# Performance work log

Measured on AMD Instinct MI355X. Metric: run time of the kernel, lower is better.

Reference implementation:

```python
import jax, jax.numpy as jnp
import numpy as np

BN_EPS = 1e-5

def _sqdist(a, b):
    # a: (B,N,3), b: (B,M,3) -> (B,N,M)
    return (jnp.sum(a**2, -1)[:, :, None] + jnp.sum(b**2, -1)[:, None, :]
            - 2.0 * jnp.einsum('bnc,bmc->bnm', a, b))

def _knn_idx(pts, k):
    # smallest-k neighbor indices, (B,N,k)
    d = _sqdist(pts, pts)
    _, idx = jax.lax.top_k(-d, k)
    return idx

def _group(feat, idx):
    # feat (B,C,N), idx (B,N,K) -> (B,C,N,K)
    return jax.vmap(lambda f, i: f[:, i])(feat, idx)

def _gather_pts(pts, idx):
    # pts (B,M,C), idx (B,...) -> (B,...,C)
    return jax.vmap(lambda p, i: p[i])(pts, idx)

def _conv1(w, b, x):
    # 1x1 conv1d: w (O,C), x (B,C,N)
    return jnp.einsum('oc,bcn->bon', w, x) + b[None, :, None]

def _conv2(w, x, b=None):
    # 1x1 conv2d: w (O,C), x (B,C,N,K)
    y = jnp.einsum('oc,bcnk->bonk', w, x)
    return y if b is None else y + b[None, :, None, None]

def _bn_eval(x, gamma, beta):
    # eval-mode BatchNorm2d with running_mean=0, running_var=1
    s = gamma / jnp.sqrt(1.0 + BN_EPS)
    return x * s[None, :, None, None] + beta[None, :, None, None]

def _lgrp(x_q, x, P_anchor, map_idx, anchor_dist, lw1, lw2, lw3, k=16):
    # x_q, x: (B,n,3) -> weights (B,dim,n,k)
    d = _sqdist(x_q, x)
    _, idx = jax.lax.top_k(-d, k)                      # (B,n,k)
    neighbors = _gather_pts(x, idx)                    # (B,n,k,3)
    R1 = jnp.abs(x_q[:, :, None, :] - neighbors)       # (B,n,k,3)
    B_idx = _gather_pts(map_idx[..., None], idx)[..., 0]  # (B,n,k)
    anchorA = _gather_pts(P_anchor, map_idx)           # (B,n,3)
    anchorB = _gather_pts(P_anchor, B_idx)             # (B,n,k,3)
    dA = jnp.linalg.norm(x_q - anchorA, axis=-1)       # (B,n)
    dB = jnp.linalg.norm(neighbors - anchorB, axis=-1) # (B,n,k)
    dAB = jax.vmap(lambda ad, a, bi: ad[a[:, None], bi])(anchor_dist, map_idx, B_idx)
    R2s = dA[:, :, None] + dAB + dB                    # (B,n,k)
    R2 = jnp.broadcast_to(R2s[..., None], R1.shape)
    feats = jnp.concatenate([R1, R2], axis=-1).transpose(0, 3, 1, 2)  # (B,6,n,k)
    h = jax.nn.relu(_conv2(lw1, feats))
    h = jax.nn.relu(_conv2(lw2, h))
    return _conv2(lw3, h)                              # (B,dim,n,k)

def setup_inputs() -> dict:
    key = jax.random.key(0)
    ks = jax.random.split(key, 32)
    B, C_in, n, dim, M, k = 2, 128, 2048, 256, 128, 16
    hid_p, hid_a = 64, dim * 4
    s = 0.05
    inp = {
        'x': jax.random.normal(ks[0], (B, C_in, n), jnp.float32),
        'pos': jax.random.normal(ks[1], (B, 3, n), jnp.float32),
        'fps_idx': jax.random.randint(ks[2], (B, n), 0, n),
        'P_anchor': jax.random.normal(ks[3], (B, M, 3), jnp.float32),
        'map_idx': jax.random.randint(ks[4], (B, n), 0, M),
        'anchor_dist': jax.random.uniform(ks[5], (B, M, M), jnp.float32) * 2.0,
        'w_start': jax.random.normal(ks[6], (dim, C_in)) * s,
        'b_start': jnp.zeros((dim,), jnp.float32),
        'w_key': jax.random.normal(ks[7], (dim, dim)) * s,
        'b_key': jnp.zeros((dim,), jnp.float32),
        'w_query': jax.random.normal(ks[8], (dim, dim)) * s,
        'b_query': jnp.zeros((dim,), jnp.float32),
        'w_value': jax.random.normal(ks[9], (dim, dim)) * s,
        'b_value': jnp.zeros((dim,), jnp.float32),
        'pw1': jax.random.normal(ks[10], (hid_p, 3)) * s,
        'pb1': jnp.zeros((hid_p,), jnp.float32),
        'pg1': jnp.ones((hid_p,), jnp.float32),
        'pbt1': jnp.zeros((hid_p,), jnp.float32),
        'pw2': jax.random.normal(ks[11], (dim, hid_p)) * s,
        'pb2': jnp.zeros((dim,), jnp.float32),
        'lw1': jax.random.normal(ks[12], (32, 6)) * s,
        'lw2': jax.random.normal(ks[13], (64, 32)) * s,
        'lw3': jax.random.normal(ks[14], (dim, 64)) * s,
        'aw1': jax.random.normal(ks[15], (hid_a, dim)) * s,
        'ab1': jnp.zeros((hid_a,), jnp.float32),
        'ag1': jnp.ones((hid_a,), jnp.float32),
        'abt1': jnp.zeros((hid_a,), jnp.float32),
        'aw2': jax.random.normal(ks[16], (dim, hid_a)) * s,
        'ab2': jnp.zeros((dim,), jnp.float32),
        'w_end': jax.random.normal(ks[17], (C_in, dim)) * s,
        'b_end': jnp.zeros((C_in,), jnp.float32),
    }
    return inp

def reference(x, pos, fps_idx, P_anchor, map_idx, anchor_dist,
              w_start, b_start, w_key, b_key, w_query, b_query, w_value, b_value,
              pw1, pb1, pg1, pbt1, pw2, pb2, lw1, lw2, lw3,
              aw1, ab1, ag1, abt1, aw2, ab2, w_end, b_end):
    n_knn = 16
    identity = x
    xf = _conv1(w_start, b_start, x)                   # (B,dim,n)
    pos_f = pos.transpose(0, 2, 1)                     # (B,n,3)
    idx_knn = _knn_idx(pos_f, n_knn)                   # (B,n,k)
    key_f = _conv1(w_key, b_key, xf)
    value = _conv1(w_value, b_value, xf)
    query = _conv1(w_query, b_query, xf)
    key_g = _group(key_f, idx_knn)                     # (B,dim,n,k)
    qk_rel = query[:, :, :, None] - key_g
    pos_rel = pos[:, :, :, None] - _group(pos, idx_knn)
    f_l = _lgrp(pos_f, pos_f, P_anchor, map_idx, anchor_dist, lw1, lw2, lw3, k=16)
    # pos_mlp: conv-bn-relu-conv
    h = _bn_eval(_conv2(pw1, pos_rel, pb1), pg1, pbt1)
    pos_emb = _conv2(pw2, jax.nn.relu(h), pb2)         # (B,dim,n,k)
    # attn_mlp
    a = _bn_eval(_conv2(aw1, qk_rel + pos_emb + f_l, ab1), ag1, abt1)
    attention = _conv2(aw2, jax.nn.relu(a), ab2)
    attention = jax.nn.softmax(attention, axis=-1)
    value_e = value[:, :, :, None] + pos_emb + f_l
    agg = jnp.sum(attention * value_e, axis=-1)        # (B,dim,n)
    y = _conv1(w_end, b_end, agg)
    return y + identity
```

## Files before the change

kernel.cpp:

```cpp
#include <hip/hip_runtime.h>
#include <hip/hip_bf16.h>

typedef __hip_bfloat16 bf16;
typedef unsigned short u16;
typedef __attribute__((ext_vector_type(8))) short s8v;
typedef __attribute__((ext_vector_type(4))) float f32x4;

#define NP    2048
#define DC    256
#define MA    128
#define KNN_  16
#define LKV   768

#define MFMA_B16(a,b,c) __builtin_amdgcn_mfma_f32_16x16x32_bf16(a,b,c,0,0,0)

__device__ __forceinline__ float u2f(u16 u){ return __uint_as_float(((unsigned int)u)<<16); }
__device__ __forceinline__ u16 f2u(float f){ bf16 h=__float2bfloat16(f); u16 us; __builtin_memcpy(&us,&h,2); return us; }

__device__ __forceinline__ s8v ldpk(const u16* pk, int rb, int KS, int ks, int l){
  return *(const s8v*)(pk + (((size_t)((rb*KS + ks)*64 + l))<<3));
}
__device__ __forceinline__ s8v ldsB(const u16* base, int col, int k0, int rshift){
  int byte = ((col<<rshift) + (k0<<1)) ^ ((col&7)<<4);
  return *(const s8v*)((const char*)base + byte);
}
__device__ __forceinline__ void st2(u16* base, int col, int ch0, int rshift,
                                    float v0, float v1, float v2, float v3){
  uint2 pkv;
  pkv.x = (unsigned)f2u(v0) | ((unsigned)f2u(v1)<<16);
  pkv.y = (unsigned)f2u(v2) | ((unsigned)f2u(v3)<<16);
  int byte = ((col<<rshift) + (ch0<<1)) ^ ((col&7)<<4);
  *(uint2*)((char*)base + byte) = pkv;
}
__device__ __forceinline__ void st1(u16* base, int col, int ch, int rshift, float v){
  int byte = ((col<<rshift) + (ch<<1)) ^ ((col&7)<<4);
  *(u16*)((char*)base + byte) = f2u(v);
}
__device__ __forceinline__ void ld4s(const u16* base, int col, int ch0, int rshift, float* o){
  int byte = ((col<<rshift) + (ch0<<1)) ^ ((col&7)<<4);
  uint2 pkv = *(const uint2*)((const char*)base + byte);
  o[0] = u2f(pkv.x & 0xffff); o[1] = u2f(pkv.x>>16);
  o[2] = u2f(pkv.y & 0xffff); o[3] = u2f(pkv.y>>16);
}

template<bool XT, bool OT, bool RES>
__global__ __launch_bounds__(256) void mgemm(
    const u16* __restrict__ apk, const float* __restrict__ X,
    const float* __restrict__ bias, const float* __restrict__ resid,
    float* __restrict__ out, int M, int N, int K, int ldo)
{
  __shared__ u16 Bt[64*256];
  const int tid = threadIdx.x;
  const int w = tid>>6, l = tid&63, k = l&15, g = l>>4;
  const int n0 = blockIdx.x*64, m0 = blockIdx.y*128, bb = blockIdx.z;
  const int KS = K >> 5;
  if constexpr (!XT) {
    for (int e = tid*4; e < 64*K; e += 1024) {
      int kk = e >> 6, c = e & 63;
      float4 v = *(const float4*)(X + (size_t)bb*K*N + (size_t)kk*N + n0 + c);
      st1(Bt, c+0, kk, 9, v.x); st1(Bt, c+1, kk, 9, v.y);
      st1(Bt, c+2, kk, 9, v.z); st1(Bt, c+3, kk, 9, v.w);
    }
  } else {
    for (int e = tid*4; e < 64*256; e += 1024) {
      int c = e >> 8, kk = e & 255;
      float4 v = *(const float4*)(X + ((size_t)bb*N + n0 + c)*256 + kk);
      st2(Bt, c, kk, 9, v.x, v.y, v.z, v.w);
    }
  }
  __syncthreads();
  f32x4 acc[2][4] = {};
  const int rbase = (m0>>4) + w*2;
  for (int ks = 0; ks < KS; ks++) {
    s8v a0 = ldpk(apk, rbase,   KS, ks, l);
    s8v a1 = ldpk(apk, rbase+1, KS, ks, l);
#pragma unroll
    for (int cf = 0; cf < 4; cf++) {
      s8v bF = ldsB(Bt, cf*16 + k, ks*32 + g*8, 9);
      acc[0][cf] = MFMA_B16(a0, bF, acc[0][cf]);
      acc[1][cf] = MFMA_B16(a1, bF, acc[1][cf]);
    }
  }
#pragma unroll
  for (int ri = 0; ri < 2; ri++) {
    int mrow = m0 + w*32 + ri*16 + g*4;
#pragma unroll
    for (int r = 0; r < 4; r++) {
      int m = mrow + r;
      float bv = bias[m];
#pragma unroll
      for (int cf = 0; cf < 4; cf++) {
        int n = n0 + cf*16 + k;
        float v = acc[ri][cf][r] + bv;
        if constexpr (RES) v += resid[((size_t)bb*M + m)*N + n];
        if constexpr (OT) out[((size_t)bb*N + n)*ldo + m] = v;
        else              out[((size_t)bb*M + m)*N + n] = v;
      }
    }
  }
}

__global__ __launch_bounds__(1024) void knn_kernel(const float* __restrict__ pos, int* __restrict__ idx)
{
  __shared__ float px[NP], py[NP], pz[NP], pn[NP];
  const int tid = threadIdx.x;
  const int w = tid >> 6, l = tid & 63;
  const int bb = blockIdx.x >> 7;
  const int q0 = (blockIdx.x & 127) * 16;
  const float* pp = pos + (size_t)bb * 3 * NP;
  for (int t = tid; t < NP; t += 1024) {
    float x = pp[t], y = pp[NP + t], z = pp[2*NP + t];
    px[t] = x; py[t] = y; pz[t] = z; pn[t] = x*x + y*y + z*z;
  }
  __syncthreads();
  const int qi = q0 + w;
  const float qx = px[qi], qy = py[qi], qz = pz[qi], qn = pn[qi];
  float bd[16]; int bi[16];
#pragma unroll
  for (int t = 0; t < 16; t++) { bd[t] = 3.4e38f; bi[t] = -1; }
  float worst = 3.4e38f;
  for (int t = 0; t < 32; t++) {
    int j = t*64 + l;
    float d = qn + pn[j] - 2.f * (qx*px[j] + qy*py[j] + qz*pz[j]);
    if (__any(d < worst)) {
      float cd = (d < worst) ? d : 3.4e38f;
      int   cj = j;
#pragma unroll
      for (int s = 0; s < 16; s++) {
        bool sw = cd < bd[s];
        float od = bd[s]; int oj = bi[s];
        bd[s] = sw ? cd : od;  bi[s] = sw ? cj : oj;
        cd    = sw ? od : cd;  cj    = sw ? oj : cj;
      }
      worst = bd[15];
    }
  }
  int myj = 0;
#pragma unroll
  for (int r = 0; r < 16; r++) {
    float md = bd[0]; int mj = bi[0];
#pragma unroll
    for (int o = 1; o < 64; o <<= 1) {
      float od = __shfl_xor(md, o);
      int   oj = __shfl_xor(mj, o);
      bool tk = (od < md) || (od == md && ((unsigned)oj < (unsigned)mj));
      md = tk ? od : md;  mj = tk ? oj : mj;
    }
    if (l == r) myj = mj;
    bool win = (bi[0] == mj);
#pragma unroll
    for (int s = 0; s < 15; s++) {
      bd[s] = win ? bd[s+1] : bd[s];
      bi[s] = win ? bi[s+1] : bi[s];
    }
    bd[15] = win ? 3.4e38f : bd[15];
  }
  if (l < 16) idx[((size_t)bb * NP + qi) * KNN_ + l] = myj;
}

__global__ __launch_bounds__(256) void prep_kernel(
    const float* __restrict__ aw1, const float* __restrict__ aw2,
    const float* __restrict__ lw3, const float* __restrict__ pw2,
    const float* __restrict__ w_start, const float* __restrict__ w_key,
    const float* __restrict__ w_query, const float* __restrict__ w_value,
    const float* __restrict__ w_end,
    const float* __restrict__ b_key, const float* __restrict__ b_query,
    const float* __restrict__ b_value,
    const float* __restrict__ ag1, const float* __restrict__ ab1, const float* __restrict__ abt1,
    const float* __restrict__ pg1, const float* __restrict__ pb1, const float* __restrict__ pbt1,
    u16* __restrict__ aw1pk, u16* __restrict__ aw2pk, u16* __restrict__ wppk,
    u16* __restrict__ wstpk, u16* __restrict__ wkqvpk, u16* __restrict__ wendpk,
    float* __restrict__ sa, float* __restrict__ oa, float* __restrict__ sp,
    float* __restrict__ op_, float* __restrict__ bkqv)
{
  int i = blockIdx.x * 256 + threadIdx.x;
  const float inv = rsqrtf(1.0f + 1e-5f);
  if (i < 262144) {
    int rb = i >> 12, rem = i & 4095, ks = rem >> 9, l = (rem >> 3) & 63, j = rem & 7;
    int row = rb*16 + (l & 15), colk = ks*32 + (l >> 4)*8 + j;
    aw1pk[i] = f2u(aw1[(size_t)row*256 + colk]); return;
  }
  i -= 262144;
  if (i < 262144) {
    int rb = i >> 14, rem = i & 16383, ks = rem >> 9, l = (rem >> 3) & 63, j = rem & 7;
    int row = rb*16 + (l & 15), colk = ks*32 + (l >> 4)*8 + j;
    aw2pk[i] = f2u(aw2[(size_t)row*1024 + colk]); return;
  }
  i -= 262144;
  if (i < 32768) {
    int rb = i >> 11, rem = i & 2047, ks = rem >> 9, l = (rem >> 3) & 63, j = rem & 7;
    int row = rb*16 + (l & 15), colk = ks*32 + (l >> 4)*8 + j;
    float v = (colk < 64) ? lw3[row*64 + colk] : pw2[row*64 + (colk - 64)];
    wppk[i] = f2u(v); return;
  }
  i -= 32768;
  if (i < 32768) {
    int rb = i >> 11, rem = i & 2047, ks = rem >> 9, l = (rem >> 3) & 63, j = rem & 7;
    int row = rb*16 + (l & 15), colk = ks*32 + (l >> 4)*8 + j;
    wstpk[i] = f2u(w_start[(size_t)row*128 + colk]); return;
  }
  i -= 32768;
  if (i < 196608) {
    int rb = i >> 12, rem = i & 4095, ks = rem >> 9, l = (rem >> 3) & 63, j = rem & 7;
    int row = rb*16 + (l & 15), colk = ks*32 + (l >> 4)*8 + j;
    float v = (row < 256) ? w_key[(size_t)row*256 + colk]
            : (row < 512) ? w_query[(size_t)(row-256)*256 + colk]
                          : w_value[(size_t)(row-512)*256 + colk];
    wkqvpk[i] = f2u(v); return;
  }
  i -= 196608;
  if (i < 32768) {
    int rb = i >> 12, rem = i & 4095, ks = rem >> 9, l = (rem >> 3) & 63, j = rem & 7;
    int row = rb*16 + (l & 15), colk = ks*32 + (l >> 4)*8 + j;
    wendpk[i] = f2u(w_end[(size_t)row*256 + colk]); return;
  }
  i -= 32768;
  if (i < 1024) { float s_ = ag1[i]*inv; sa[i] = s_; oa[i] = ab1[i]*s_ + abt1[i]; return; }
  i -= 1024;
  if (i < 64)  { float s_ = pg1[i]*inv; sp[i] = s_; op_[i] = pb1[i]*s_ + pbt1[i]; return; }
  i -= 64;
  if (i < 768) {
    bkqv[i] = (i < 256) ? b_key[i] : (i < 512) ? b_query[i-256] : b_value[i-512];
  }
}

__global__ __launch_bounds__(256, 2) void fused_attn(
    const float* __restrict__ kqv, const int* __restrict__ knn_idx,
    const float* __restrict__ pos, const int* __restrict__ map_idx,
    const float* __restrict__ P_anchor, const float* __restrict__ adist,
    const float* __restrict__ lw1f, const float* __restrict__ lw2f, const float* __restrict__ pw1f,
    const float* __restrict__ spv, const float* __restrict__ opv, const float* __restrict__ pb2f,
    const u16* __restrict__ aw1pk, const float* __restrict__ sav, const float* __restrict__ oav,
    const u16* __restrict__ aw2pk, const u16* __restrict__ wppk, const float* __restrict__ ab2f,
    float* __restrict__ aggT)
{
  __shared__ __align__(16) char smem[49152];
  u16*   s_t   = (u16*)smem;
  u16*   hid_t = (u16*)(smem + 32768);
  float* fFEAT = (float*)smem;
  float* fPREL = (float*)(smem + 1632);
  u16*   fH1   = (u16*) (smem + 2448);
  __shared__ int s_idx[4][16];

  const int tid = threadIdx.x;
  const int w = tid >> 6, l = tid & 63;
  const int k = l & 15, g = l >> 4;
  const int p0 = blockIdx.x * 4;
  const int b = p0 >> 11, pi0 = p0 & 2047;
  const int pi = pi0 + w;
  const int col_w = w*16 + k;

  const float* kqvB = kqv + (size_t)b * NP * LKV;

  if (l < 16) {
    int kk = l;
    int j = knn_idx[((size_t)(b*NP) + pi) * KNN_ + kk];
    s_idx[w][kk] = j;
    const float* pp = pos + (size_t)b * 3 * NP;
    float qx = pp[pi], qy = pp[NP+pi], qz = pp[2*NP+pi];
    float nx = pp[j],  ny = pp[NP+j],  nz = pp[2*NP+j];
    float r1x = qx-nx, r1y = qy-ny, r1z = qz-nz;
    fPREL[(w*3+0)*17+kk] = r1x; fPREL[(w*3+1)*17+kk] = r1y; fPREL[(w*3+2)*17+kk] = r1z;
    int mi = map_idx[b*NP + pi];
    int bj = map_idx[b*NP + j];
    const float* pa = P_anchor + (size_t)b * MA * 3;
    float ax = pa[mi*3], ay = pa[mi*3+1], az = pa[mi*3+2];
    float bx = pa[bj*3], by = pa[bj*3+1], bz = pa[bj*3+2];
    float dA = sqrtf((qx-ax)*(qx-ax)+(qy-ay)*(qy-ay)+(qz-az)*(qz-az));
    float dB = sqrtf((nx-bx)*(nx-bx)+(ny-by)*(ny-by)+(nz-bz)*(nz-bz));
    float dAB = adist[(size_t)b*MA*MA + mi*MA + bj];
    float r2 = dA + dAB + dB;
    fFEAT[(w*6+0)*17+kk] = fabsf(r1x); fFEAT[(w*6+1)*17+kk] = fabsf(r1y);
    fFEAT[(w*6+2)*17+kk] = fabsf(r1z);
    fFEAT[(w*6+3)*17+kk] = r2; fFEAT[(w*6+4)*17+kk] = r2; fFEAT[(w*6+5)*17+kk] = r2;
  }
  __syncthreads();

  {
    float f0=fFEAT[(w*6+0)*17+k], f1=fFEAT[(w*6+1)*17+k], f2=fFEAT[(w*6+2)*17+k],
          f3=fFEAT[(w*6+3)*17+k], f4=fFEAT[(w*6+4)*17+k], f5=fFEAT[(w*6+5)*17+k];
#pragma unroll
    for (int jj = 0; jj < 8; jj++) {
      int h = g*8 + jj;
      const float* wp = lw1f + h*6;
      float v = wp[0]*f0 + wp[1]*f1 + wp[2]*f2 + wp[3]*f3 + wp[4]*f4 + wp[5]*f5;
      fH1[(w*32+h)*17+k] = f2u(fmaxf(v, 0.f));
    }
  }
  __syncthreads();

  {
    float hr[32];
#pragma unroll
    for (int t = 0; t < 32; t++) hr[t] = u2f(fH1[(w*32+t)*17+k]);
#pragma unroll
    for (int jj = 0; jj < 16; jj++) {
      int h = g*16 + jj;
      const float4* wp = (const float4*)(lw2f + h*32);
      float a = 0.f;
#pragma unroll
      for (int t4 = 0; t4 < 8; t4++) {
        float4 wv = wp[t4];
        a += wv.x*hr[t4*4] + wv.y*hr[t4*4+1] + wv.z*hr[t4*4+2] + wv.w*hr[t4*4+3];
      }
      st1(hid_t, col_w, h, 8, fmaxf(a, 0.f));
    }
    float pr0 = fPREL[(w*3+0)*17+k], pr1 = fPREL[(w*3+1)*17+k], pr2 = fPREL[(w*3+2)*17+k];
#pragma unroll
    for (int jj = 0; jj < 16; jj++) {
      int h = g*16 + jj;
      float d = pw1f[h*3]*pr0 + pw1f[h*3+1]*pr1 + pw1f[h*3+2]*pr2;
      st1(hid_t, col_w, 64 + h, 8, fmaxf(d*spv[h] + opv[h], 0.f));
    }
  }
  __syncthreads();

  {
    f32x4 accs[4][4];
#pragma unroll
    for (int fr = 0; fr < 4; fr++) {
      int ch0 = w*64 + fr*16 + g*4;
      const float4 p4 = *(const float4*)(pb2f + ch0);
#pragma unroll
      for (int fc = 0; fc < 4; fc++) {
        int j = s_idx[fc][k];
        const float4 q4 = *(const float4*)(kqvB + (size_t)(pi0 + fc)*LKV + 256 + ch0);
        const float4 k4 = *(const float4*)(kqvB + (size_t)j*LKV + ch0);
        accs[fr][fc][0] = q4.x - k4.x + p4.x;
        accs[fr][fc][1] = q4.y - k4.y + p4.y;
        accs[fr][fc][2] = q4.z - k4.z + p4.z;
        accs[fr][fc][3] = q4.w - k4.w + p4.w;
      }
    }
#pragma unroll
    for (int ks = 0; ks < 4; ks++) {
      s8v aF[4];
#pragma unroll
      for (int fr = 0; fr < 4; fr++) aF[fr] = ldpk(wppk, w*4 + fr, 4, ks, l);
#pragma unroll
      for (int fc = 0; fc < 4; fc++) {
        s8v bF = ldsB(hid_t, fc*16 + k, ks*32 + g*8, 8);
#pragma unroll
        for (int fr = 0; fr < 4; fr++) accs[fr][fc] = MFMA_B16(aF[fr], bF, accs[fr][fc]);
      }
    }
#pragma unroll
    for (int fr = 0; fr < 4; fr++)
#pragma unroll
      for (int fc = 0; fc < 4; fc++)
        st2(s_t, fc*16 + k, w*64 + fr*16 + g*4, 9,
            accs[fr][fc][0], accs[fr][fc][1], accs[fr][fc][2], accs[fr][fc][3]);
  }
  __syncthreads();

  f32x4 acc2[4][4];
#pragma unroll
  for (int fr = 0; fr < 4; fr++) {
    const float4 a4 = *(const float4*)(ab2f + w*64 + fr*16 + g*4);
#pragma unroll
    for (int fc = 0; fc < 4; fc++) {
      acc2[fr][fc][0] = a4.x; acc2[fr][fc][1] = a4.y;
      acc2[fr][fc][2] = a4.z; acc2[fr][fc][3] = a4.w;
    }
  }

  for (int c = 0; c < 8; c++) {
    f32x4 acc1[2][4] = {};
    int rb0 = c*8 + w*2;
#pragma unroll
    for (int ks = 0; ks < 8; ks++) {
      s8v a0 = ldpk(aw1pk, rb0,     8, ks, l);
      s8v a1 = ldpk(aw1pk, rb0 + 1, 8, ks, l);
#pragma unroll
      for (int cf = 0; cf < 4; cf++) {
        s8v bF = ldsB(s_t, cf*16 + k, ks*32 + g*8, 9);
        acc1[0][cf] = MFMA_B16(a0, bF, acc1[0][cf]);
        acc1[1][cf] = MFMA_B16(a1, bF, acc1[1][cf]);
      }
    }
    __syncthreads();
#pragma unroll
    for (int ri = 0; ri < 2; ri++) {
      int hl = w*32 + ri*16 + g*4;
      int hg = c*128 + hl;
      const float4 sc = *(const float4*)(sav + hg);
      const float4 of = *(const float4*)(oav + hg);
#pragma unroll
      for (int cf = 0; cf < 4; cf++) {
        float v0 = fmaxf(acc1[ri][cf][0]*sc.x + of.x, 0.f);
        float v1 = fmaxf(acc1[ri][cf][1]*sc.y + of.y, 0.f);
        float v2 = fmaxf(acc1[ri][cf][2]*sc.z + of.z, 0.f);
        float v3 = fmaxf(acc1[ri][cf][3]*sc.w + of.w, 0.f);
        st2(hid_t, cf*16 + k, hl, 8, v0, v1, v2, v3);
      }
    }
    __syncthreads();
#pragma unroll
    for (int ks = 0; ks < 4; ks++) {
      s8v aF[4];
#pragma unroll
      for (int rf = 0; rf < 4; rf++) aF[rf] = ldpk(aw2pk, w*4 + rf, 32, c*4 + ks, l);
#pragma unroll
      for (int cf = 0; cf < 4; cf++) {
        s8v bF = ldsB(hid_t, cf*16 + k, ks*32 + g*8, 8);
#pragma unroll
        for (int rf = 0; rf < 4; rf++) acc2[rf][cf] = MFMA_B16(aF[rf], bF, acc2[rf][cf]);
      }
    }
  }

#pragma unroll
  for (int fc = 0; fc < 4; fc++) {
    int j = s_idx[fc][k];
    const float* qp = kqvB + (size_t)(pi0 + fc)*LKV + 256;
    const float* kp = kqvB + (size_t)j*LKV;
    const float* vp = kqvB + (size_t)(pi0 + fc)*LKV + 512;
#pragma unroll
    for (int fr = 0; fr < 4; fr++) {
      int ch0 = w*64 + fr*16 + g*4;
      float q4[4], k4[4], v4[4], s4[4], res[4];
      *(float4*)q4 = *(const float4*)(qp + ch0);
      *(float4*)k4 = *(const float4*)(kp + ch0);
      *(float4*)v4 = *(const float4*)(vp + ch0);
      ld4s(s_t, fc*16 + k, ch0, 9, s4);
#pragma unroll
      for (int r = 0; r < 4; r++) {
        float a = acc2[fr][fc][r];
        float m = a;
        m = fmaxf(m, __shfl_xor(m, 1, 16)); m = fmaxf(m, __shfl_xor(m, 2, 16));
        m = fmaxf(m, __shfl_xor(m, 4, 16)); m = fmaxf(m, __shfl_xor(m, 8, 16));
        float ex = __expf(a - m);
        float se = ex;
        se += __shfl_xor(se, 1, 16); se += __shfl_xor(se, 2, 16);
        se += __shfl_xor(se, 4, 16); se += __shfl_xor(se, 8, 16);
        float watt = ex / se;
        float ve = v4[r] - q4[r] + k4[r] + s4[r];
        float cc = watt * ve;
        cc += __shfl_xor(cc, 1, 16); cc += __shfl_xor(cc, 2, 16);
        cc += __shfl_xor(cc, 4, 16); cc += __shfl_xor(cc, 8, 16);
        res[r] = cc;
      }
      if (k == 0)
        *(float4*)(aggT + ((size_t)(b*NP) + pi0 + fc)*DC + ch0) =
            make_float4(res[0], res[1], res[2], res[3]);
    }
  }
}

extern "C" void kernel_launch(void* const* d_in, const int* in_sizes, int n_in,
                              void* d_out, int out_size, void* d_ws, size_t ws_size,
                              hipStream_t stream)
{
  const float* x        = (const float*)d_in[0];
  const float* pos      = (const float*)d_in[1];
  const float* P_anchor = (const float*)d_in[3];
  const int*   map_idx  = (const int*)  d_in[4];
  const float* adist    = (const float*)d_in[5];
  const float* w_start  = (const float*)d_in[6];
  const float* b_start  = (const float*)d_in[7];
  const float* w_key    = (const float*)d_in[8];
  const float* b_key    = (const float*)d_in[9];
  const float* w_query  = (const float*)d_in[10];
  const float* b_query  = (const float*)d_in[11];
  const float* w_value  = (const float*)d_in[12];
  const float* b_value  = (const float*)d_in[13];
  const float* pw1      = (const float*)d_in[14];
  const float* pb1      = (const float*)d_in[15];
  const float* pg1      = (const float*)d_in[16];
  const float* pbt1     = (const float*)d_in[17];
  const float* pw2      = (const float*)d_in[18];
  const float* pb2      = (const float*)d_in[19];
  const float* lw1      = (const float*)d_in[20];
  const float* lw2      = (const float*)d_in[21];
  const float* lw3      = (const float*)d_in[22];
  const float* aw1      = (const float*)d_in[23];
  const float* ab1      = (const float*)d_in[24];
  const float* ag1      = (const float*)d_in[25];
  const float* abt1     = (const float*)d_in[26];
  const float* aw2      = (const float*)d_in[27];
  const float* ab2      = (const float*)d_in[28];
  const float* w_end    = (const float*)d_in[29];
  const float* b_end    = (const float*)d_in[30];

  if (ws_size < (size_t)4672384 * 4) return;

  float* ws     = (float*)d_ws;
  float* xf     = ws + 0;
  float* aggT   = ws + 0;
  float* kqvT   = ws + 1048576;
  u16*   aw1pk  = (u16*)(ws + 4194304);
  u16*   aw2pk  = (u16*)(ws + 4325376);
  u16*   wppk   = (u16*)(ws + 4456448);
  u16*   wstpk  = (u16*)(ws + 4472832);
  u16*   wkqvpk = (u16*)(ws + 4489216);
  u16*   wendpk = (u16*)(ws + 4587520);
  float* sa     = ws + 4603904;
  float* oa     = ws + 4604928;
  float* sp     = ws + 4605952;
  float* op_    = ws + 4606016;
  float* bkqv   = ws + 4606080;
  int*   knn_i  = (int*)(ws + 4606848);

  prep_kernel<<<3208, 256, 0, stream>>>(aw1, aw2, lw3, pw2,
      w_start, w_key, w_query, w_value, w_end, b_key, b_query, b_value,
      ag1, ab1, abt1, pg1, pb1, pbt1,
      aw1pk, aw2pk, wppk, wstpk, wkqvpk, wendpk, sa, oa, sp, op_, bkqv);

  mgemm<false, false, false><<<dim3(32, 2, 2), 256, 0, stream>>>(
      wstpk, x, b_start, nullptr, xf, 256, NP, 128, 0);

  knn_kernel<<<256, 1024, 0, stream>>>(pos, knn_i);

  mgemm<false, true, false><<<dim3(32, 6, 2), 256, 0, stream>>>(
      wkqvpk, xf, bkqv, nullptr, kqvT, 768, NP, 256, LKV);

  fused_attn<<<1024, 256, 0, stream>>>(kqvT, knn_i,
      pos, map_idx, P_anchor, adist,
      lw1, lw2, pw1, sp, op_, pb2,
      aw1pk, sa, oa, aw2pk, wppk, ab2, aggT);

  mgemm<true, false, true><<<dim3(32, 1, 2), 256, 0, stream>>>(
      wendpk, aggT, b_end, x, (float*)d_out, 128, NP, 256, 0);
}
```

Baseline: 241.9 us.

## Shrink LDS footprint by halving hidden tile and splitting pos-MLP staging

The hidden LDS buffer shrinks from 128 to 64 columns of width: the lgrp hidden and the pos_mlp hidden are now staged one after another with an extra barrier, and the attn_mlp chunk loop runs 16 chunks of 64 instead of 8 of 128. The shared knn index array is dropped and indices are reloaded from global memory. Total LDS falls from 48KB plus the index array to 40KB, which could let more blocks fit per CU. The cost is twice as many barriers in the main loop, less A-fragment reuse per MFMA step, and extra global index loads.

```diff
diff --git a/kernel.cpp b/kernel.cpp
--- a/kernel.cpp
+++ b/kernel.cpp
@@ -234,13 +234,12 @@
     const u16* __restrict__ aw2pk, const u16* __restrict__ wppk, const float* __restrict__ ab2f,
     float* __restrict__ aggT)
 {
-  __shared__ __align__(16) char smem[49152];
+  __shared__ __align__(16) char smem[40960];
   u16*   s_t   = (u16*)smem;
   u16*   hid_t = (u16*)(smem + 32768);
   float* fFEAT = (float*)smem;
   float* fPREL = (float*)(smem + 1632);
   u16*   fH1   = (u16*) (smem + 2448);
-  __shared__ int s_idx[4][16];
 
   const int tid = threadIdx.x;
   const int w = tid >> 6, l = tid & 63;
@@ -251,11 +250,11 @@
   const int col_w = w*16 + k;
 
   const float* kqvB = kqv + (size_t)b * NP * LKV;
+  const int* knnB = knn_idx + ((size_t)b * NP) * KNN_;
 
   if (l < 16) {
     int kk = l;
-    int j = knn_idx[((size_t)(b*NP) + pi) * KNN_ + kk];
-    s_idx[w][kk] = j;
+    int j = knnB[(size_t)pi * KNN_ + kk];
     const float* pp = pos + (size_t)b * 3 * NP;
     float qx = pp[pi], qy = pp[NP+pi], qz = pp[2*NP+pi];
     float nx = pp[j],  ny = pp[NP+j],  nz = pp[2*NP+j];
@@ -303,27 +302,20 @@
         float4 wv = wp[t4];
         a += wv.x*hr[t4*4] + wv.y*hr[t4*4+1] + wv.z*hr[t4*4+2] + wv.w*hr[t4*4+3];
       }
-      st1(hid_t, col_w, h, 8, fmaxf(a, 0.f));
-    }
-    float pr0 = fPREL[(w*3+0)*17+k], pr1 = fPREL[(w*3+1)*17+k], pr2 = fPREL[(w*3+2)*17+k];
-#pragma unroll
-    for (int jj = 0; jj < 16; jj++) {
-      int h = g*16 + jj;
-      float d = pw1f[h*3]*pr0 + pw1f[h*3+1]*pr1 + pw1f[h*3+2]*pr2;
-      st1(hid_t, col_w, 64 + h, 8, fmaxf(d*spv[h] + opv[h], 0.f));
-    }
-  }
-  __syncthreads();
-
+      st1(hid_t, col_w, h, 7, fmaxf(a, 0.f));
+    }
+  }
+  __syncthreads();
+
+  f32x4 accs[4][4];
   {
-    f32x4 accs[4][4];
 #pragma unroll
     for (int fr = 0; fr < 4; fr++) {
       int ch0 = w*64 + fr*16 + g*4;
       const float4 p4 = *(const float4*)(pb2f + ch0);
 #pragma unroll
       for (int fc = 0; fc < 4; fc++) {
-        int j = s_idx[fc][k];
+        int j = knnB[(size_t)(pi0 + fc) * KNN_ + k];
         const float4 q4 = *(const float4*)(kqvB + (size_t)(pi0 + fc)*LKV + 256 + ch0);
         const float4 k4 = *(const float4*)(kqvB + (size_t)j*LKV + ch0);
         accs[fr][fc][0] = q4.x - k4.x + p4.x;
@@ -333,13 +325,40 @@
       }
     }
 #pragma unroll
-    for (int ks = 0; ks < 4; ks++) {
+    for (int ks = 0; ks < 2; ks++) {
       s8v aF[4];
 #pragma unroll
       for (int fr = 0; fr < 4; fr++) aF[fr] = ldpk(wppk, w*4 + fr, 4, ks, l);
 #pragma unroll
       for (int fc = 0; fc < 4; fc++) {
-        s8v bF = ldsB(hid_t, fc*16 + k, ks*32 + g*8, 8);
+        s8v bF = ldsB(hid_t, fc*16 + k, ks*32 + g*8, 7);
+#pragma unroll
+        for (int fr = 0; fr < 4; fr++) accs[fr][fc] = MFMA_B16(aF[fr], bF, accs[fr][fc]);
+      }
+    }
+  }
+  __syncthreads();
+
+  {
+    float pr0 = fPREL[(w*3+0)*17+k], pr1 = fPREL[(w*3+1)*17+k], pr2 = fPREL[(w*3+2)*17+k];
+#pragma unroll
+    for (int jj = 0; jj < 16; jj++) {
+      int h = g*16 + jj;
+      float d = pw1f[h*3]*pr0 + pw1f[h*3+1]*pr1 + pw1f[h*3+2]*pr2;
+      st1(hid_t, col_w, h, 7, fmaxf(d*spv[h] + opv[h], 0.f));
+    }
+  }
+  __syncthreads();
+
+  {
+#pragma unroll
+    for (int ks = 0; ks < 2; ks++) {
+      s8v aF[4];
+#pragma unroll
+      for (int fr = 0; fr < 4; fr++) aF[fr] = ldpk(wppk, w*4 + fr, 4, 2 + ks, l);
+#pragma unroll
+      for (int fc = 0; fc < 4; fc++) {
+        s8v bF = ldsB(hid_t, fc*16 + k, ks*32 + g*8, 7);
 #pragma unroll
         for (int fr = 0; fr < 4; fr++) accs[fr][fc] = MFMA_B16(aF[fr], bF, accs[fr][fc]);
       }
@@ -364,45 +383,42 @@
     }
   }
 
-  for (int c = 0; c < 8; c++) {
-    f32x4 acc1[2][4] = {};
-    int rb0 = c*8 + w*2;
+  for (int c = 0; c < 16; c++) {
+    f32x4 acc1[4] = {};
+    const int rb = c*4 + w;
 #pragma unroll
     for (int ks = 0; ks < 8; ks++) {
-      s8v a0 = ldpk(aw1pk, rb0,     8, ks, l);
-      s8v a1 = ldpk(aw1pk, rb0 + 1, 8, ks, l);
+      s8v a0 = ldpk(aw1pk, rb, 8, ks, l);
 #pragma unroll
       for (int cf = 0; cf < 4; cf++) {
         s8v bF = ldsB(s_t, cf*16 + k, ks*32 + g*8, 9);
-        acc1[0][cf] = MFMA_B16(a0, bF, acc1[0][cf]);
-        acc1[1][cf] = MFMA_B16(a1, bF, acc1[1][cf]);
+        acc1[cf] = MFMA_B16(a0, bF, acc1[cf]);
       }
     }
     __syncthreads();
-#pragma unroll
-    for (int ri = 0; ri < 2; ri++) {
-      int hl = w*32 + ri*16 + g*4;
-      int hg = c*128 + hl;
+    {
+      int hl = w*16 + g*4;
+      int hg = rb*16 + g*4;
       const float4 sc = *(const float4*)(sav + hg);
       const float4 of = *(const float4*)(oav + hg);
 #pragma unroll
       for (int cf = 0; cf < 4; cf++) {
-        float v0 = fmaxf(acc1[ri][cf][0]*sc.x + of.x, 0.f);
-        float v1 = fmaxf(acc1[ri][cf][1]*sc.y + of.y, 0.f);
-        float v2 = fmaxf(acc1[ri][cf][2]*sc.z + of.z, 0.f);
-        float v3 = fmaxf(acc1[ri][cf][3]*sc.w + of.w, 0.f);
-        st2(hid_t, cf*16 + k, hl, 8, v0, v1, v2, v3);
+        float v0 = fmaxf(acc1[cf][0]*sc.x + of.x, 0.f);
+        float v1 = fmaxf(acc1[cf][1]*sc.y + of.y, 0.f);
+        float v2 = fmaxf(acc1[cf][2]*sc.z + of.z, 0.f);
+        float v3 = fmaxf(acc1[cf][3]*sc.w + of.w, 0.f);
+        st2(hid_t, cf*16 + k, hl, 7, v0, v1, v2, v3);
       }
     }
     __syncthreads();
 #pragma unroll
-    for (int ks = 0; ks < 4; ks++) {
+    for (int ks = 0; ks < 2; ks++) {
       s8v aF[4];
 #pragma unroll
-      for (int rf = 0; rf < 4; rf++) aF[rf] = ldpk(aw2pk, w*4 + rf, 32, c*4 + ks, l);
+      for (int rf = 0; rf < 4; rf++) aF[rf] = ldpk(aw2pk, w*4 + rf, 32, c*2 + ks, l);
 #pragma unroll
       for (int cf = 0; cf < 4; cf++) {
-        s8v bF = ldsB(hid_t, cf*16 + k, ks*32 + g*8, 8);
+        s8v bF = ldsB(hid_t, cf*16 + k, ks*32 + g*8, 7);
 #pragma unroll
         for (int rf = 0; rf < 4; rf++) acc2[rf][cf] = MFMA_B16(aF[rf], bF, acc2[rf][cf]);
       }
@@ -411,7 +427,7 @@
 
 #pragma unroll
   for (int fc = 0; fc < 4; fc++) {
-    int j = s_idx[fc][k];
+    int j = knnB[(size_t)(pi0 + fc) * KNN_ + k];
     const float* qp = kqvB + (size_t)(pi0 + fc)*LKV + 256;
     const float* kp = kqvB + (size_t)j*LKV;
     const float* vp = kqvB + (size_t)(pi0 + fc)*LKV + 512;
```

New measurement: 234.8 us. 1.03x faster.

## Switch fused attention MLP GEMMs to 32x32x16 bf16 MFMA tiles

Applied to the files above, without the earlier changes.

Repacks the aw1, aw2 and lw3/pw2 weights for the 32x32x16 MFMA operand layout and rewrites all three in-kernel GEMMs to use 32x32 tiles. Each wave now computes 2x2 32x32 fragments instead of 4x4 16x16 ones, which cuts the MFMA instruction count and the B-operand LDS reads per FLOP. The hidden chunk grows to 256 rows per outer iteration (4 iterations instead of 8), so the hidden LDS buffer doubles and shared memory rises to 64KB. Neighbor indices are reread from global memory instead of a shared array. The larger LDS footprint may reduce the number of blocks resident per CU.

```diff
diff --git a/kernel.cpp b/kernel.cpp
--- a/kernel.cpp
+++ b/kernel.cpp
@@ -5,6 +5,7 @@
 typedef unsigned short u16;
 typedef __attribute__((ext_vector_type(8))) short s8v;
 typedef __attribute__((ext_vector_type(4))) float f32x4;
+typedef __attribute__((ext_vector_type(16))) float f32x16;
 
 #define NP    2048
 #define DC    256
@@ -13,6 +14,7 @@
 #define LKV   768
 
 #define MFMA_B16(a,b,c) __builtin_amdgcn_mfma_f32_16x16x32_bf16(a,b,c,0,0,0)
+#define MFMA32(a,b,c)   __builtin_amdgcn_mfma_f32_32x32x16_bf16(a,b,c,0,0,0)
 
 __device__ __forceinline__ float u2f(u16 u){ return __uint_as_float(((unsigned int)u)<<16); }
 __device__ __forceinline__ u16 f2u(float f){ bf16 h=__float2bfloat16(f); u16 us; __builtin_memcpy(&us,&h,2); return us; }
@@ -176,20 +178,20 @@
   int i = blockIdx.x * 256 + threadIdx.x;
   const float inv = rsqrtf(1.0f + 1e-5f);
   if (i < 262144) {
-    int rb = i >> 12, rem = i & 4095, ks = rem >> 9, l = (rem >> 3) & 63, j = rem & 7;
-    int row = rb*16 + (l & 15), colk = ks*32 + (l >> 4)*8 + j;
+    int j = i & 7, l = (i >> 3) & 63, ks = (i >> 9) & 15, rb = i >> 13;
+    int row = rb*32 + (l & 31), colk = ks*16 + (l >> 5)*8 + j;
     aw1pk[i] = f2u(aw1[(size_t)row*256 + colk]); return;
   }
   i -= 262144;
   if (i < 262144) {
-    int rb = i >> 14, rem = i & 16383, ks = rem >> 9, l = (rem >> 3) & 63, j = rem & 7;
-    int row = rb*16 + (l & 15), colk = ks*32 + (l >> 4)*8 + j;
+    int j = i & 7, l = (i >> 3) & 63, ks = (i >> 9) & 63, rb = i >> 15;
+    int row = rb*32 + (l & 31), colk = ks*16 + (l >> 5)*8 + j;
     aw2pk[i] = f2u(aw2[(size_t)row*1024 + colk]); return;
   }
   i -= 262144;
   if (i < 32768) {
-    int rb = i >> 11, rem = i & 2047, ks = rem >> 9, l = (rem >> 3) & 63, j = rem & 7;
-    int row = rb*16 + (l & 15), colk = ks*32 + (l >> 4)*8 + j;
+    int j = i & 7, l = (i >> 3) & 63, ks = (i >> 9) & 7, rb = i >> 12;
+    int row = rb*32 + (l & 31), colk = ks*16 + (l >> 5)*8 + j;
     float v = (colk < 64) ? lw3[row*64 + colk] : pw2[row*64 + (colk - 64)];
     wppk[i] = f2u(v); return;
   }
@@ -234,28 +236,28 @@
     const u16* __restrict__ aw2pk, const u16* __restrict__ wppk, const float* __restrict__ ab2f,
     float* __restrict__ aggT)
 {
-  __shared__ __align__(16) char smem[49152];
+  __shared__ __align__(16) char smem[65536];
   u16*   s_t   = (u16*)smem;
   u16*   hid_t = (u16*)(smem + 32768);
   float* fFEAT = (float*)smem;
   float* fPREL = (float*)(smem + 1632);
   u16*   fH1   = (u16*) (smem + 2448);
-  __shared__ int s_idx[4][16];
 
   const int tid = threadIdx.x;
   const int w = tid >> 6, l = tid & 63;
   const int k = l & 15, g = l >> 4;
+  const int c32 = l & 31, h = l >> 5;
   const int p0 = blockIdx.x * 4;
   const int b = p0 >> 11, pi0 = p0 & 2047;
   const int pi = pi0 + w;
   const int col_w = w*16 + k;
 
   const float* kqvB = kqv + (size_t)b * NP * LKV;
+  const int* knnB = knn_idx + ((size_t)b * NP) * KNN_;
 
   if (l < 16) {
     int kk = l;
-    int j = knn_idx[((size_t)(b*NP) + pi) * KNN_ + kk];
-    s_idx[w][kk] = j;
+    int j = knnB[(size_t)pi * KNN_ + kk];
     const float* pp = pos + (size_t)b * 3 * NP;
     float qx = pp[pi], qy = pp[NP+pi], qz = pp[2*NP+pi];
     float nx = pp[j],  ny = pp[NP+j],  nz = pp[2*NP+j];
@@ -281,10 +283,10 @@
           f3=fFEAT[(w*6+3)*17+k], f4=fFEAT[(w*6+4)*17+k], f5=fFEAT[(w*6+5)*17+k];
 #pragma unroll
     for (int jj = 0; jj < 8; jj++) {
-      int h = g*8 + jj;
-      const float* wp = lw1f + h*6;
+      int hh = g*8 + jj;
+      const float* wp = lw1f + hh*6;
       float v = wp[0]*f0 + wp[1]*f1 + wp[2]*f2 + wp[3]*f3 + wp[4]*f4 + wp[5]*f5;
-      fH1[(w*32+h)*17+k] = f2u(fmaxf(v, 0.f));
+      fH1[(w*32+hh)*17+k] = f2u(fmaxf(v, 0.f));
     }
   }
   __syncthreads();
@@ -295,137 +297,152 @@
     for (int t = 0; t < 32; t++) hr[t] = u2f(fH1[(w*32+t)*17+k]);
 #pragma unroll
     for (int jj = 0; jj < 16; jj++) {
-      int h = g*16 + jj;
-      const float4* wp = (const float4*)(lw2f + h*32);
+      int hh = g*16 + jj;
+      const float4* wp = (const float4*)(lw2f + hh*32);
       float a = 0.f;
 #pragma unroll
       for (int t4 = 0; t4 < 8; t4++) {
         float4 wv = wp[t4];
         a += wv.x*hr[t4*4] + wv.y*hr[t4*4+1] + wv.z*hr[t4*4+2] + wv.w*hr[t4*4+3];
       }
-      st1(hid_t, col_w, h, 8, fmaxf(a, 0.f));
+      st1(hid_t, col_w, hh, 9, fmaxf(a, 0.f));
     }
     float pr0 = fPREL[(w*3+0)*17+k], pr1 = fPREL[(w*3+1)*17+k], pr2 = fPREL[(w*3+2)*17+k];
 #pragma unroll
     for (int jj = 0; jj < 16; jj++) {
-      int h = g*16 + jj;
-      float d = pw1f[h*3]*pr0 + pw1f[h*3+1]*pr1 + pw1f[h*3+2]*pr2;
-      st1(hid_t, col_w, 64 + h, 8, fmaxf(d*spv[h] + opv[h], 0.f));
+      int hh = g*16 + jj;
+      float d = pw1f[hh*3]*pr0 + pw1f[hh*3+1]*pr1 + pw1f[hh*3+2]*pr2;
+      st1(hid_t, col_w, 64 + hh, 9, fmaxf(d*spv[hh] + opv[hh], 0.f));
     }
   }
   __syncthreads();
 
   {
-    f32x4 accs[4][4];
-#pragma unroll
-    for (int fr = 0; fr < 4; fr++) {
-      int ch0 = w*64 + fr*16 + g*4;
-      const float4 p4 = *(const float4*)(pb2f + ch0);
-#pragma unroll
-      for (int fc = 0; fc < 4; fc++) {
-        int j = s_idx[fc][k];
-        const float4 q4 = *(const float4*)(kqvB + (size_t)(pi0 + fc)*LKV + 256 + ch0);
-        const float4 k4 = *(const float4*)(kqvB + (size_t)j*LKV + ch0);
-        accs[fr][fc][0] = q4.x - k4.x + p4.x;
-        accs[fr][fc][1] = q4.y - k4.y + p4.y;
-        accs[fr][fc][2] = q4.z - k4.z + p4.z;
-        accs[fr][fc][3] = q4.w - k4.w + p4.w;
-      }
-    }
-#pragma unroll
-    for (int ks = 0; ks < 4; ks++) {
-      s8v aF[4];
-#pragma unroll
-      for (int fr = 0; fr < 4; fr++) aF[fr] = ldpk(wppk, w*4 + fr, 4, ks, l);
-#pragma unroll
-      for (int fc = 0; fc < 4; fc++) {
-        s8v bF = ldsB(hid_t, fc*16 + k, ks*32 + g*8, 8);
-#pragma unroll
-        for (int fr = 0; fr < 4; fr++) accs[fr][fc] = MFMA_B16(aF[fr], bF, accs[fr][fc]);
-      }
-    }
-#pragma unroll
-    for (int fr = 0; fr < 4; fr++)
-#pragma unroll
-      for (int fc = 0; fc < 4; fc++)
-        st2(s_t, fc*16 + k, w*64 + fr*16 + g*4, 9,
-            accs[fr][fc][0], accs[fr][fc][1], accs[fr][fc][2], accs[fr][fc][3]);
+    f32x16 accs[2][2];
+#pragma unroll
+    for (int fr = 0; fr < 2; fr++)
+#pragma unroll
+    for (int fc = 0; fc < 2; fc++) {
+      int p = fc*2 + (c32 >> 4), kk = c32 & 15;
+      int j = knnB[(size_t)(pi0 + p)*KNN_ + kk];
+      const float* qrow = kqvB + (size_t)(pi0 + p)*LKV + 256;
+      const float* krow = kqvB + (size_t)j*LKV;
+#pragma unroll
+      for (int q = 0; q < 4; q++) {
+        int ch0 = w*64 + fr*32 + q*8 + 4*h;
+        float4 q4 = *(const float4*)(qrow + ch0);
+        float4 k4 = *(const float4*)(krow + ch0);
+        float4 p4 = *(const float4*)(pb2f + ch0);
+        accs[fr][fc][q*4+0] = q4.x - k4.x + p4.x;
+        accs[fr][fc][q*4+1] = q4.y - k4.y + p4.y;
+        accs[fr][fc][q*4+2] = q4.z - k4.z + p4.z;
+        accs[fr][fc][q*4+3] = q4.w - k4.w + p4.w;
+      }
+    }
+#pragma unroll
+    for (int ks = 0; ks < 8; ks++) {
+      s8v a0 = ldpk(wppk, w*2 + 0, 8, ks, l);
+      s8v a1 = ldpk(wppk, w*2 + 1, 8, ks, l);
+#pragma unroll
+      for (int fc = 0; fc < 2; fc++) {
+        s8v bF = ldsB(hid_t, fc*32 + c32, ks*16 + h*8, 9);
+        accs[0][fc] = MFMA32(a0, bF, accs[0][fc]);
+        accs[1][fc] = MFMA32(a1, bF, accs[1][fc]);
+      }
+    }
+#pragma unroll
+    for (int fr = 0; fr < 2; fr++)
+#pragma unroll
+    for (int fc = 0; fc < 2; fc++)
+#pragma unroll
+      for (int q = 0; q < 4; q++)
+        st2(s_t, fc*32 + c32, w*64 + fr*32 + q*8 + 4*h, 9,
+            accs[fr][fc][q*4+0], accs[fr][fc][q*4+1],
+            accs[fr][fc][q*4+2], accs[fr][fc][q*4+3]);
   }
   __syncthreads();
 
-  f32x4 acc2[4][4];
-#pragma unroll
-  for (int fr = 0; fr < 4; fr++) {
-    const float4 a4 = *(const float4*)(ab2f + w*64 + fr*16 + g*4);
-#pragma unroll
-    for (int fc = 0; fc < 4; fc++) {
-      acc2[fr][fc][0] = a4.x; acc2[fr][fc][1] = a4.y;
-      acc2[fr][fc][2] = a4.z; acc2[fr][fc][3] = a4.w;
-    }
-  }
-
-  for (int c = 0; c < 8; c++) {
-    f32x4 acc1[2][4] = {};
-    int rb0 = c*8 + w*2;
-#pragma unroll
-    for (int ks = 0; ks < 8; ks++) {
-      s8v a0 = ldpk(aw1pk, rb0,     8, ks, l);
-      s8v a1 = ldpk(aw1pk, rb0 + 1, 8, ks, l);
-#pragma unroll
-      for (int cf = 0; cf < 4; cf++) {
-        s8v bF = ldsB(s_t, cf*16 + k, ks*32 + g*8, 9);
-        acc1[0][cf] = MFMA_B16(a0, bF, acc1[0][cf]);
-        acc1[1][cf] = MFMA_B16(a1, bF, acc1[1][cf]);
+  f32x16 acc2[2][2];
+#pragma unroll
+  for (int fr = 0; fr < 2; fr++)
+#pragma unroll
+  for (int fc = 0; fc < 2; fc++)
+#pragma unroll
+    for (int q = 0; q < 4; q++) {
+      int ch0 = w*64 + fr*32 + q*8 + 4*h;
+      float4 a4 = *(const float4*)(ab2f + ch0);
+      acc2[fr][fc][q*4+0] = a4.x; acc2[fr][fc][q*4+1] = a4.y;
+      acc2[fr][fc][q*4+2] = a4.z; acc2[fr][fc][q*4+3] = a4.w;
+    }
+
+  for (int c = 0; c < 4; c++) {
+    f32x16 acc1[2][2] = {};
+    const int rb0 = c*8 + w, rb1 = rb0 + 4;
+#pragma unroll
+    for (int ks = 0; ks < 16; ks++) {
+      s8v a0 = ldpk(aw1pk, rb0, 16, ks, l);
+      s8v a1 = ldpk(aw1pk, rb1, 16, ks, l);
+#pragma unroll
+      for (int fc = 0; fc < 2; fc++) {
+        s8v bF = ldsB(s_t, fc*32 + c32, ks*16 + h*8, 9);
+        acc1[0][fc] = MFMA32(a0, bF, acc1[0][fc]);
+        acc1[1][fc] = MFMA32(a1, bF, acc1[1][fc]);
       }
     }
     __syncthreads();
 #pragma unroll
     for (int ri = 0; ri < 2; ri++) {
-      int hl = w*32 + ri*16 + g*4;
-      int hg = c*128 + hl;
-      const float4 sc = *(const float4*)(sav + hg);
-      const float4 of = *(const float4*)(oav + hg);
-#pragma unroll
-      for (int cf = 0; cf < 4; cf++) {
-        float v0 = fmaxf(acc1[ri][cf][0]*sc.x + of.x, 0.f);
-        float v1 = fmaxf(acc1[ri][cf][1]*sc.y + of.y, 0.f);
-        float v2 = fmaxf(acc1[ri][cf][2]*sc.z + of.z, 0.f);
-        float v3 = fmaxf(acc1[ri][cf][3]*sc.w + of.w, 0.f);
-        st2(hid_t, cf*16 + k, hl, 8, v0, v1, v2, v3);
+      const int rbg = c*8 + w + ri*4;
+#pragma unroll
+      for (int q = 0; q < 4; q++) {
+        int hg0 = rbg*32 + q*8 + 4*h;
+        float4 sc = *(const float4*)(sav + hg0);
+        float4 of = *(const float4*)(oav + hg0);
+        int hl0 = (w + ri*4)*32 + q*8 + 4*h;
+#pragma unroll
+        for (int fc = 0; fc < 2; fc++) {
+          float v0 = fmaxf(acc1[ri][fc][q*4+0]*sc.x + of.x, 0.f);
+          float v1 = fmaxf(acc1[ri][fc][q*4+1]*sc.y + of.y, 0.f);
+          float v2 = fmaxf(acc1[ri][fc][q*4+2]*sc.z + of.z, 0.f);
+          float v3 = fmaxf(acc1[ri][fc][q*4+3]*sc.w + of.w, 0.f);
+          st2(hid_t, fc*32 + c32, hl0, 9, v0, v1, v2, v3);
+        }
       }
     }
     __syncthreads();
 #pragma unroll
-    for (int ks = 0; ks < 4; ks++) {
-      s8v aF[4];
-#pragma unroll
-      for (int rf = 0; rf < 4; rf++) aF[rf] = ldpk(aw2pk, w*4 + rf, 32, c*4 + ks, l);
-#pragma unroll
-      for (int cf = 0; cf < 4; cf++) {
-        s8v bF = ldsB(hid_t, cf*16 + k, ks*32 + g*8, 8);
-#pragma unroll
-        for (int rf = 0; rf < 4; rf++) acc2[rf][cf] = MFMA_B16(aF[rf], bF, acc2[rf][cf]);
-      }
-    }
-  }
-
-#pragma unroll
-  for (int fc = 0; fc < 4; fc++) {
-    int j = s_idx[fc][k];
-    const float* qp = kqvB + (size_t)(pi0 + fc)*LKV + 256;
+    for (int ks = 0; ks < 16; ks++) {
+      s8v a0 = ldpk(aw2pk, w*2 + 0, 64, c*16 + ks, l);
+      s8v a1 = ldpk(aw2pk, w*2 + 1, 64, c*16 + ks, l);
+#pragma unroll
+      for (int fc = 0; fc < 2; fc++) {
+        s8v bF = ldsB(hid_t, fc*32 + c32, ks*16 + h*8, 9);
+        acc2[0][fc] = MFMA32(a0, bF, acc2[0][fc]);
+        acc2[1][fc] = MFMA32(a1, bF, acc2[1][fc]);
+      }
+    }
+  }
+
+#pragma unroll
+  for (int fr = 0; fr < 2; fr++)
+#pragma unroll
+  for (int fc = 0; fc < 2; fc++) {
+    int p = fc*2 + (c32 >> 4), kk = c32 & 15;
+    int j = knnB[(size_t)(pi0 + p)*KNN_ + kk];
+    const float* qp = kqvB + (size_t)(pi0 + p)*LKV + 256;
     const float* kp = kqvB + (size_t)j*LKV;
-    const float* vp = kqvB + (size_t)(pi0 + fc)*LKV + 512;
-#pragma unroll
-    for (int fr = 0; fr < 4; fr++) {
-      int ch0 = w*64 + fr*16 + g*4;
+    const float* vp = kqvB + (size_t)(pi0 + p)*LKV + 512;
+#pragma unroll
+    for (int q = 0; q < 4; q++) {
+      int ch0 = w*64 + fr*32 + q*8 + 4*h;
       float q4[4], k4[4], v4[4], s4[4], res[4];
       *(float4*)q4 = *(const float4*)(qp + ch0);
       *(float4*)k4 = *(const float4*)(kp + ch0);
       *(float4*)v4 = *(const float4*)(vp + ch0);
-      ld4s(s_t, fc*16 + k, ch0, 9, s4);
+      ld4s(s_t, fc*32 + c32, ch0, 9, s4);
 #pragma unroll
       for (int r = 0; r < 4; r++) {
-        float a = acc2[fr][fc][r];
+        float a = acc2[fr][fc][q*4+r];
         float m = a;
         m = fmaxf(m, __shfl_xor(m, 1, 16)); m = fmaxf(m, __shfl_xor(m, 2, 16));
         m = fmaxf(m, __shfl_xor(m, 4, 16)); m = fmaxf(m, __shfl_xor(m, 8, 16));
@@ -440,8 +457,8 @@
         cc += __shfl_xor(cc, 4, 16); cc += __shfl_xor(cc, 8, 16);
         res[r] = cc;
       }
-      if (k == 0)
-        *(float4*)(aggT + ((size_t)(b*NP) + pi0 + fc)*DC + ch0) =
+      if (kk == 0)
+        *(float4*)(aggT + ((size_t)(b*NP) + pi0 + p)*DC + ch0) =
             make_float4(res[0], res[1], res[2], res[3]);
     }
   }
```

New measurement: 273.5 us. +13.1%, slower.

## Double-buffer attention hidden tile to halve barriers in the MLP chunk loop

Applied to the files above, without the earlier changes.

Adds a second LDS hidden buffer so the aw2 MFMA pass over chunk c reads one buffer while the aw1 pass for chunk c+1 writes the other. This cuts the loop to one barrier per chunk instead of two and lets the two GEMM stages interleave. It also drops the shared s_idx array and reloads knn indices from global memory. LDS use grows from 48KB to 64KB per block, which may reduce occupancy given launch_bounds(256,2).

```diff
diff --git a/kernel.cpp b/kernel.cpp
--- a/kernel.cpp
+++ b/kernel.cpp
@@ -234,13 +234,13 @@
     const u16* __restrict__ aw2pk, const u16* __restrict__ wppk, const float* __restrict__ ab2f,
     float* __restrict__ aggT)
 {
-  __shared__ __align__(16) char smem[49152];
+  __shared__ __align__(16) char smem[65536];
   u16*   s_t   = (u16*)smem;
-  u16*   hid_t = (u16*)(smem + 32768);
+  u16*   hid0  = (u16*)(smem + 32768);
+  u16*   hid1  = (u16*)(smem + 49152);
   float* fFEAT = (float*)smem;
   float* fPREL = (float*)(smem + 1632);
   u16*   fH1   = (u16*) (smem + 2448);
-  __shared__ int s_idx[4][16];
 
   const int tid = threadIdx.x;
   const int w = tid >> 6, l = tid & 63;
@@ -251,11 +251,11 @@
   const int col_w = w*16 + k;
 
   const float* kqvB = kqv + (size_t)b * NP * LKV;
+  const int* knnB = knn_idx + ((size_t)b * NP) * KNN_;
 
   if (l < 16) {
     int kk = l;
-    int j = knn_idx[((size_t)(b*NP) + pi) * KNN_ + kk];
-    s_idx[w][kk] = j;
+    int j = knnB[(size_t)pi * KNN_ + kk];
     const float* pp = pos + (size_t)b * 3 * NP;
     float qx = pp[pi], qy = pp[NP+pi], qz = pp[2*NP+pi];
     float nx = pp[j],  ny = pp[NP+j],  nz = pp[2*NP+j];
@@ -303,14 +303,14 @@
         float4 wv = wp[t4];
         a += wv.x*hr[t4*4] + wv.y*hr[t4*4+1] + wv.z*hr[t4*4+2] + wv.w*hr[t4*4+3];
       }
-      st1(hid_t, col_w, h, 8, fmaxf(a, 0.f));
+      st1(hid0, col_w, h, 8, fmaxf(a, 0.f));
     }
     float pr0 = fPREL[(w*3+0)*17+k], pr1 = fPREL[(w*3+1)*17+k], pr2 = fPREL[(w*3+2)*17+k];
 #pragma unroll
     for (int jj = 0; jj < 16; jj++) {
       int h = g*16 + jj;
       float d = pw1f[h*3]*pr0 + pw1f[h*3+1]*pr1 + pw1f[h*3+2]*pr2;
-      st1(hid_t, col_w, 64 + h, 8, fmaxf(d*spv[h] + opv[h], 0.f));
+      st1(hid0, col_w, 64 + h, 8, fmaxf(d*spv[h] + opv[h], 0.f));
     }
   }
   __syncthreads();
@@ -323,7 +323,7 @@
       const float4 p4 = *(const float4*)(pb2f + ch0);
 #pragma unroll
       for (int fc = 0; fc < 4; fc++) {
-        int j = s_idx[fc][k];
+        int j = knnB[(size_t)(pi0 + fc) * KNN_ + k];
         const float4 q4 = *(const float4*)(kqvB + (size_t)(pi0 + fc)*LKV + 256 + ch0);
         const float4 k4 = *(const float4*)(kqvB + (size_t)j*LKV + ch0);
         accs[fr][fc][0] = q4.x - k4.x + p4.x;
@@ -339,7 +339,7 @@
       for (int fr = 0; fr < 4; fr++) aF[fr] = ldpk(wppk, w*4 + fr, 4, ks, l);
 #pragma unroll
       for (int fc = 0; fc < 4; fc++) {
-        s8v bF = ldsB(hid_t, fc*16 + k, ks*32 + g*8, 8);
+        s8v bF = ldsB(hid0, fc*16 + k, ks*32 + g*8, 8);
 #pragma unroll
         for (int fr = 0; fr < 4; fr++) accs[fr][fc] = MFMA_B16(aF[fr], bF, accs[fr][fc]);
       }
@@ -364,9 +364,9 @@
     }
   }
 
-  for (int c = 0; c < 8; c++) {
+  {
     f32x4 acc1[2][4] = {};
-    int rb0 = c*8 + w*2;
+    const int rb0 = w*2;
 #pragma unroll
     for (int ks = 0; ks < 8; ks++) {
       s8v a0 = ldpk(aw1pk, rb0,     8, ks, l);
@@ -378,23 +378,26 @@
         acc1[1][cf] = MFMA_B16(a1, bF, acc1[1][cf]);
       }
     }
-    __syncthreads();
 #pragma unroll
     for (int ri = 0; ri < 2; ri++) {
       int hl = w*32 + ri*16 + g*4;
-      int hg = c*128 + hl;
-      const float4 sc = *(const float4*)(sav + hg);
-      const float4 of = *(const float4*)(oav + hg);
+      const float4 sc = *(const float4*)(sav + hl);
+      const float4 of = *(const float4*)(oav + hl);
 #pragma unroll
       for (int cf = 0; cf < 4; cf++) {
         float v0 = fmaxf(acc1[ri][cf][0]*sc.x + of.x, 0.f);
         float v1 = fmaxf(acc1[ri][cf][1]*sc.y + of.y, 0.f);
         float v2 = fmaxf(acc1[ri][cf][2]*sc.z + of.z, 0.f);
         float v3 = fmaxf(acc1[ri][cf][3]*sc.w + of.w, 0.f);
-        st2(hid_t, cf*16 + k, hl, 8, v0, v1, v2, v3);
-      }
-    }
-    __syncthreads();
+        st2(hid0, cf*16 + k, hl, 8, v0, v1, v2, v3);
+      }
+    }
+  }
+  __syncthreads();
+
+  for (int c = 0; c < 8; c++) {
+    u16* cur = (c & 1) ? hid1 : hid0;
+    u16* nxt = (c & 1) ? hid0 : hid1;
 #pragma unroll
     for (int ks = 0; ks < 4; ks++) {
       s8v aF[4];
@@ -402,16 +405,47 @@
       for (int rf = 0; rf < 4; rf++) aF[rf] = ldpk(aw2pk, w*4 + rf, 32, c*4 + ks, l);
 #pragma unroll
       for (int cf = 0; cf < 4; cf++) {
-        s8v bF = ldsB(hid_t, cf*16 + k, ks*32 + g*8, 8);
+        s8v bF = ldsB(cur, cf*16 + k, ks*32 + g*8, 8);
 #pragma unroll
         for (int rf = 0; rf < 4; rf++) acc2[rf][cf] = MFMA_B16(aF[rf], bF, acc2[rf][cf]);
       }
     }
+    if (c < 7) {
+      f32x4 acc1[2][4] = {};
+      const int rb0 = (c+1)*8 + w*2;
+#pragma unroll
+      for (int ks = 0; ks < 8; ks++) {
+        s8v a0 = ldpk(aw1pk, rb0,     8, ks, l);
+        s8v a1 = ldpk(aw1pk, rb0 + 1, 8, ks, l);
+#pragma unroll
+        for (int cf = 0; cf < 4; cf++) {
+          s8v bF = ldsB(s_t, cf*16 + k, ks*32 + g*8, 9);
+          acc1[0][cf] = MFMA_B16(a0, bF, acc1[0][cf]);
+          acc1[1][cf] = MFMA_B16(a1, bF, acc1[1][cf]);
+        }
+      }
+#pragma unroll
+      for (int ri = 0; ri < 2; ri++) {
+        int hl = w*32 + ri*16 + g*4;
+        int hg = (c+1)*128 + hl;
+        const float4 sc = *(const float4*)(sav + hg);
+        const float4 of = *(const float4*)(oav + hg);
+#pragma unroll
+        for (int cf = 0; cf < 4; cf++) {
+          float v0 = fmaxf(acc1[ri][cf][0]*sc.x + of.x, 0.f);
+          float v1 = fmaxf(acc1[ri][cf][1]*sc.y + of.y, 0.f);
+          float v2 = fmaxf(acc1[ri][cf][2]*sc.z + of.z, 0.f);
+          float v3 = fmaxf(acc1[ri][cf][3]*sc.w + of.w, 0.f);
+          st2(nxt, cf*16 + k, hl, 8, v0, v1, v2, v3);
+        }
+      }
+      __syncthreads();
+    }
   }
 
 #pragma unroll
   for (int fc = 0; fc < 4; fc++) {
-    int j = s_idx[fc][k];
+    int j = knnB[(size_t)(pi0 + fc) * KNN_ + k];
     const float* qp = kqvB + (size_t)(pi0 + fc)*LKV + 256;
     const float* kp = kqvB + (size_t)j*LKV;
     const float* vp = kqvB + (size_t)(pi0 + fc)*LKV + 512;
```

Measured after the change: 233.6 us. 3.4% less time.
